# Kernel optimization log

Measured on AMD Instinct MI355X. Metric: run time of the kernel, lower is better.

## Reference

```python
import jax, jax.numpy as jnp
import numpy as np

NUM_NODES = 100
WINDOW = 128
GH = 256       # graph_hidden_channels
DH = 64        # discrepancy_hidden_channels
OUT = 128      # out_channels
B = 256        # graphs per batch
N = B * NUM_NODES
E = 409600


def _mconv(x, w, b):
    # x: [B, n, W], w: [n, 2, k], b: [n, 2]  (per-node Conv1d(1,2,k), 'same' padding)
    k = w.shape[-1]
    W = x.shape[-1]
    p = k // 2
    xp = jnp.pad(x, ((0, 0), (0, 0), (p, p)))
    win = jnp.stack([xp[..., j:j + W] for j in range(k)], axis=-1)  # [B,n,W,k]
    return jnp.einsum('bnwk,nck->bncw', win, w) + b[None, :, :, None]


def _gcn(x, edge_index, Wg, bg):
    # PyG GCNConv: add self-loops, symmetric normalization, then linear
    Nn = x.shape[0]
    xw = x @ Wg.T
    loops = jnp.arange(Nn, dtype=edge_index.dtype)
    src = jnp.concatenate([edge_index[0], loops])
    dst = jnp.concatenate([edge_index[1], loops])
    deg = jax.ops.segment_sum(jnp.ones(src.shape[0], dtype=xw.dtype), dst, num_segments=Nn)
    norm = jax.lax.rsqrt(jnp.maximum(deg, 1e-12))
    coef = norm[src] * norm[dst]
    agg = jax.ops.segment_sum(coef[:, None] * xw[src], dst, num_segments=Nn)
    return agg + bg


def setup_inputs() -> dict:
    key = jax.random.key(0)
    ks = jax.random.split(key, 20)
    f = 6 * WINDOW
    s = lambda d: 1.0 / np.sqrt(d)
    inp = {
        'x1': jax.random.normal(ks[0], (N, WINDOW), jnp.float32),
        'x2': jax.random.normal(ks[1], (N, WINDOW), jnp.float32),
        'edge_index1': jax.random.randint(ks[2], (2, E), 0, N, jnp.int32),
        'edge_index2': jax.random.randint(ks[3], (2, E), 0, N, jnp.int32),
        'w3': jax.random.normal(ks[4], (NUM_NODES, 2, 3), jnp.float32) * s(3),
        'b3': jax.random.normal(ks[5], (NUM_NODES, 2), jnp.float32) * s(3),
        'w5': jax.random.normal(ks[6], (NUM_NODES, 2, 5), jnp.float32) * s(5),
        'b5': jax.random.normal(ks[7], (NUM_NODES, 2), jnp.float32) * s(5),
        'w7': jax.random.normal(ks[8], (NUM_NODES, 2, 7), jnp.float32) * s(7),
        'b7': jax.random.normal(ks[9], (NUM_NODES, 2), jnp.float32) * s(7),
        'Wff': jax.random.normal(ks[10], (NUM_NODES, GH, f), jnp.float32) * s(f),
        'bff': jax.random.normal(ks[11], (NUM_NODES, GH), jnp.float32) * s(f),
        'Wg': jax.random.normal(ks[12], (GH, GH), jnp.float32) * s(GH),
        'bg': jax.random.normal(ks[13], (GH,), jnp.float32) * s(GH),
        'Wd': jax.random.normal(ks[14], (NUM_NODES, DH, 2 * GH), jnp.float32) * s(2 * GH),
        'bd': jax.random.normal(ks[15], (NUM_NODES, DH), jnp.float32) * s(2 * GH),
        'Wfc': jax.random.normal(ks[16], (OUT, NUM_NODES * DH), jnp.float32) * s(NUM_NODES * DH),
        'bfc': jax.random.normal(ks[17], (OUT,), jnp.float32) * s(NUM_NODES * DH),
    }
    return inp


def reference(x1, x2, edge_index1, edge_index2, w3, b3, w5, b5, w7, b7,
              Wff, bff, Wg, bg, Wd, bd, Wfc, bfc):
    n = w3.shape[0]
    Nn, W = x1.shape
    Bg = Nn // n

    def branch(x):
        xg = x.reshape(Bg, n, W)
        # multiscale CNN: concat conv3/conv5/conv7 along channel -> [B,n,6,W]
        c = jnp.concatenate([_mconv(xg, w3, b3), _mconv(xg, w5, b5), _mconv(xg, w7, b7)], axis=2)
        c = jax.nn.relu(c.reshape(Bg, n, 6 * W))            # channel-major flatten (matches view(-1))
        h = jax.nn.relu(jnp.einsum('bnf,nhf->bnh', c, Wff) + bff)
        return h.reshape(Nn, -1)

    h1 = jax.nn.relu(_gcn(branch(x1), edge_index1, Wg, bg))
    h2 = jax.nn.relu(_gcn(branch(x2), edge_index2, Wg, bg))
    H = h1.shape[-1]
    cat = jnp.concatenate([h1.reshape(Bg, n, H), h2.reshape(Bg, n, H)], axis=-1)  # [B,n,2H]
    d = jnp.einsum('bnf,ndf->bnd', cat, Wd) + bd            # per-node discrepancy FC
    du = jax.nn.relu(d.reshape(Bg, -1))                     # node-major -> [B, n*DH]
    return du @ Wfc.T + bfc
```

## Files before the change

kernel.cpp:

```cpp
#include <hip/hip_runtime.h>

#define DI __device__ __forceinline__

typedef __bf16 bf16_t;
typedef bf16_t bf16x8 __attribute__((ext_vector_type(8)));
typedef float f32x4 __attribute__((ext_vector_type(4)));
typedef ushort ushort8v __attribute__((ext_vector_type(8)));

static constexpr int NNODE = 100, WIN = 128, GH = 256, DH = 64, OUTC = 128, NB = 256;
static constexpr int NTOT = NB * NNODE;
static constexpr int NE = 409600;
static constexpr int FFK = 6 * WIN;
static constexpr size_t CB = (size_t)NNODE * NB * FFK;
static constexpr size_t HB = (size_t)NTOT * GH;
static constexpr int CVT_BLKS = 23264;

DI ushort f2bf(float f) {
  union { float f; unsigned u; } v; v.f = f;
  unsigned r = v.u + 0x7fffu + ((v.u >> 16) & 1u);
  return (ushort)(r >> 16);
}
DI float bf2f(ushort s) {
  union { unsigned u; float f; } v; v.u = ((unsigned)s) << 16; return v.f;
}

DI void gload16(const void* g, void* l) {
  __builtin_amdgcn_global_load_lds((const __attribute__((address_space(1))) void*)g,
                                   (__attribute__((address_space(3))) void*)l, 16, 0, 0);
}


DI void cvt_body(int bx, const float* s0, const float* s1, const float* s2, const float* s3,
                 ushort* d0, ushort* d1, ushort* d2, ushort* d3) {
  int j = bx * 256 + threadIdx.x;
  const float* s; ushort* d;
  if (j < 19660800 / 4) { s = s0; d = d0; }
  else if ((j -= 19660800 / 4) < 3276800 / 4) { s = s1; d = d1; }
  else if ((j -= 3276800 / 4) < 819200 / 4) { s = s2; d = d2; }
  else { j -= 819200 / 4; s = s3; d = d3; }
  float4 v = reinterpret_cast<const float4*>(s)[j];
  ushort4 o;
  o.x = f2bf(v.x); o.y = f2bf(v.y); o.z = f2bf(v.z); o.w = f2bf(v.w);
  reinterpret_cast<ushort4*>(d)[j] = o;
}

DI void hist_body(int bx, const int* d1, const int* d2, int* deg, int* rank) {
  int i = bx * 256 + threadIdx.x;
  if (i < NE) rank[i] = atomicAdd(&deg[d1[i]], 1);
  else if (i < 2 * NE) rank[i] = atomicAdd(&deg[NTOT + d2[i - NE]], 1);
}

DI void fill_body(int bx, const int* e1, const int* e2, const int* offs,
                  const int* rank, int* csr) {
  int i = bx * 256 + threadIdx.x;
  if (i < NE) {
    int d = e1[NE + i];
    csr[offs[d] + rank[i]] = e1[i];
  } else if (i < 2 * NE) {
    int ii = i - NE;
    int d = e2[NE + ii];
    csr[NE + offs[NTOT + 1 + d] + rank[i]] = e2[ii];
  }
}

DI void scan_body(int set, const int* deg_, int* offs_, float* norm_) {
  const int* deg = deg_ + set * NTOT;
  int* offs = offs_ + set * (NTOT + 1);
  float* norm = norm_ + set * NTOT;
  __shared__ int part[256];
  int t = threadIdx.x;
  int base = t * 100;
  int s = 0;
  for (int j = 0; j < 100; ++j) s += deg[base + j];
  part[t] = s;
  __syncthreads();
  for (int d = 1; d < 256; d <<= 1) {
    int vv = (t >= d) ? part[t - d] : 0;
    __syncthreads();
    part[t] += vv;
    __syncthreads();
  }
  int run = (t > 0) ? part[t - 1] : 0;
  for (int j = 0; j < 100; ++j) {
    int dv = deg[base + j];
    offs[base + j] = run;
    norm[base + j] = rsqrtf((float)(dv + 1));
    run += dv;
  }
  if (t == 255) offs[NTOT] = part[255];
}

DI void conv_body(int bx, const float* x1, const float* x2,
                  const float* w3, const float* b3, const float* w5, const float* b5,
                  const float* w7, const float* b7, ushort* c) {
  const int t = threadIdx.x;
  const int rowi = t >> 4;
  const int idx = t & 15;
  int r = bx * 16 + rowi;
  int br = r >= NTOT;
  int rr = r - br * NTOT;
  const float* x = br ? x2 : x1;
  int b = rr / 100, node = rr - b * 100;

  __shared__ float xs[16][136];
  const int w0 = idx * 8;
  float4 v0 = *reinterpret_cast<const float4*>(x + (size_t)rr * WIN + w0);
  float4 v1 = *reinterpret_cast<const float4*>(x + (size_t)rr * WIN + w0 + 4);
  *reinterpret_cast<float4*>(&xs[rowi][4 + w0]) = v0;
  *reinterpret_cast<float4*>(&xs[rowi][4 + w0 + 4]) = v1;
  if (idx == 0) { xs[rowi][0] = 0.f; xs[rowi][1] = 0.f; xs[rowi][2] = 0.f; xs[rowi][3] = 0.f; }
  if (idx == 15) { xs[rowi][132] = 0.f; xs[rowi][133] = 0.f; xs[rowi][134] = 0.f; xs[rowi][135] = 0.f; }
  __syncthreads();

  float xv[14];
#pragma unroll
  for (int j = 0; j < 14; ++j) xv[j] = xs[rowi][1 + w0 + j];

  const float* W3 = w3 + node * 6;  const float* B3 = b3 + node * 2;
  const float* W5 = w5 + node * 10; const float* B5 = b5 + node * 2;
  const float* W7 = w7 + node * 14; const float* B7 = b7 + node * 2;
  ushort* out = c + (size_t)br * CB + (size_t)(node * NB + b) * FFK + w0;

#pragma unroll
  for (int ch = 0; ch < 2; ++ch) {
    float k3[3], k5[5], k7[7];
#pragma unroll
    for (int j = 0; j < 3; ++j) k3[j] = W3[ch * 3 + j];
#pragma unroll
    for (int j = 0; j < 5; ++j) k5[j] = W5[ch * 5 + j];
#pragma unroll
    for (int j = 0; j < 7; ++j) k7[j] = W7[ch * 7 + j];
    float bb3 = B3[ch], bb5 = B5[ch], bb7 = B7[ch];
    ushort8v o3, o5, o7;
#pragma unroll
    for (int p = 0; p < 8; ++p) {
      float a3 = bb3, a5 = bb5, a7 = bb7;
#pragma unroll
      for (int j = 0; j < 3; ++j) a3 += k3[j] * xv[p + 2 + j];
#pragma unroll
      for (int j = 0; j < 5; ++j) a5 += k5[j] * xv[p + 1 + j];
#pragma unroll
      for (int j = 0; j < 7; ++j) a7 += k7[j] * xv[p + j];
      o3[p] = f2bf(fmaxf(a3, 0.f));
      o5[p] = f2bf(fmaxf(a5, 0.f));
      o7[p] = f2bf(fmaxf(a7, 0.f));
    }
    *reinterpret_cast<ushort8v*>(out + (0 + ch) * WIN) = o3;
    *reinterpret_cast<ushort8v*>(out + (2 + ch) * WIN) = o5;
    *reinterpret_cast<ushort8v*>(out + (4 + ch) * WIN) = o7;
  }
}

template <int MODE>
DI void gemm_body(int bx, int by, const ushort* __restrict__ A, const ushort* __restrict__ A2,
                  const ushort* __restrict__ Bm, ushort* __restrict__ obf,
                  float* __restrict__ of, const float* __restrict__ bias) {
  constexpr int BN = (MODE == 2) ? 64 : 128;
  constexpr int KT = (MODE == 0) ? 12 : (MODE == 1) ? 4 : (MODE == 2) ? 8 : 4;
  constexpr int LDA = (MODE == 0) ? 768 : (MODE == 1) ? 256 : (MODE == 2) ? 256 : 6400;
  constexpr int LDB = (MODE == 0) ? 768 : (MODE == 1) ? 256 : (MODE == 2) ? 512 : 6400;
  constexpr int MF = (MODE == 2) ? 2 : 4;
  constexpr int NF = 4;

  __shared__ ushort As[128 * 64];
  __shared__ ushort Bs[BN * 64];

  const int tid = threadIdx.x, wv = tid >> 6, lane = tid & 63;
  const int j8 = (((lane & 7) ^ (lane >> 3)) - (lane & 7)) * 8;

  int mt = 0, nt = 0, node = 0, kbase = 0, br = 0;
  if constexpr (MODE == 0) {
    int h = bx;
    int s = (h & 7) * 100 + (h >> 3);
    nt = s & 1; int rest = s >> 1;
    mt = rest & 1; int yy = rest >> 1;
    br = yy >= 100; node = yy - br * 100;
  } else if constexpr (MODE == 1) {
    int h = bx;
    int s = (h & 7) * 100 + (h >> 3);
    nt = s & 1; int rest = s >> 1;
    br = rest >= 200; mt = rest - br * 200;
  } else if constexpr (MODE == 2) { mt = bx; node = by; }
  else { mt = bx; kbase = by * 256; }

  const ushort* Ab = nullptr; const ushort* Bb = nullptr;
  if constexpr (MODE == 0) { Ab = A + (size_t)br * CB + (size_t)node * (NB * FFK) + (size_t)mt * 128 * FFK;
                             Bb = Bm + (size_t)node * (GH * FFK) + (size_t)nt * 128 * FFK; }
  else if constexpr (MODE == 1) { Ab = A + (size_t)br * HB + (size_t)mt * 128 * GH;
                                  Bb = Bm + (size_t)nt * 128 * GH; }
  else if constexpr (MODE == 2) { Bb = Bm + (size_t)node * (DH * 512); }
  else { Ab = A + (size_t)mt * 128 * 6400 + kbase; Bb = Bm + kbase; }

  const int wr = (MODE == 2) ? wv : (wv >> 1);
  const int wc = (MODE == 2) ? 0 : (wv & 1);

  f32x4 acc[MF][NF] = {};

  for (int kt = 0; kt < KT; ++kt) {
    const int k0 = kt * 64;
    __syncthreads();
#pragma unroll
    for (int it = 0; it < 4; ++it) {
      int rb = it * 32 + wv * 8;
      int row = rb + (lane >> 3);
      const ushort* gp;
      if constexpr (MODE == 2) {
        int b_ = mt * 128 + row;
        const ushort* src = (k0 < 256) ? A : A2;
        gp = src + (size_t)(b_ * NNODE + node) * GH + (k0 & 255) + (lane & 7) * 8 + j8;
      } else {
        gp = Ab + (size_t)row * LDA + k0 + (lane & 7) * 8 + j8;
      }
      gload16(gp, &As[rb * 64]);
    }
#pragma unroll
    for (int it = 0; it < BN / 32; ++it) {
      int rb = it * 32 + wv * 8;
      int row = rb + (lane >> 3);
      gload16(Bb + (size_t)row * LDB + k0 + (lane & 7) * 8 + j8, &Bs[rb * 64]);
    }
    __syncthreads();
#pragma unroll
    for (int kk = 0; kk < 2; ++kk) {
      const int ch8 = ((kk * 4 + (lane >> 4)) ^ (lane & 7)) * 8;
      bf16x8 af[MF], bfr[NF];
#pragma unroll
      for (int m = 0; m < MF; ++m) {
        int rr = wr * (MF * 16) + m * 16 + (lane & 15);
        af[m] = *reinterpret_cast<const bf16x8*>(&As[rr * 64 + ch8]);
      }
#pragma unroll
      for (int n = 0; n < NF; ++n) {
        int rr = wc * 64 + n * 16 + (lane & 15);
        bfr[n] = *reinterpret_cast<const bf16x8*>(&Bs[rr * 64 + ch8]);
      }
#pragma unroll
      for (int m = 0; m < MF; ++m)
#pragma unroll
        for (int n = 0; n < NF; ++n)
          acc[m][n] = __builtin_amdgcn_mfma_f32_16x16x32_bf16(af[m], bfr[n], acc[m][n], 0, 0, 0);
    }
  }

  const int lrow = (lane >> 4) * 4, lcol = lane & 15;
#pragma unroll
  for (int m = 0; m < MF; ++m) {
#pragma unroll
    for (int n = 0; n < NF; ++n) {
      int cc = wc * 64 + n * 16 + lcol;
#pragma unroll
      for (int rg = 0; rg < 4; ++rg) {
        int rr = wr * (MF * 16) + m * 16 + lrow + rg;
        float val = acc[m][n][rg];
        if constexpr (MODE == 0) {
          int b_ = mt * 128 + rr;
          int col = nt * 128 + cc;
          val = fmaxf(val + bias[node * GH + col], 0.f);
          obf[(size_t)br * HB + (size_t)(b_ * NNODE + node) * GH + col] = f2bf(val);
        } else if constexpr (MODE == 1) {
          int R = mt * 128 + rr;
          int col = nt * 128 + cc;
          obf[(size_t)br * HB + (size_t)R * GH + col] = f2bf(val * bias[br * NTOT + R]);
        } else if constexpr (MODE == 2) {
          int b_ = mt * 128 + rr;
          val = fmaxf(val + bias[node * DH + cc], 0.f);
          obf[(size_t)b_ * (NNODE * DH) + node * DH + cc] = f2bf(val);
        } else {
          int R = mt * 128 + rr;
          if (by == 0) val += bias[cc];
          atomicAdd(&of[R * OUTC + cc], val);
        }
      }
    }
  }
}


__global__ __launch_bounds__(256) void fused1_k(
    const float* __restrict__ Wff, const float* __restrict__ Wd,
    const float* __restrict__ Wfc, const float* __restrict__ Wg,
    ushort* __restrict__ Wffb, ushort* __restrict__ Wdb,
    ushort* __restrict__ Wfcb, ushort* __restrict__ Wgb,
    const int* __restrict__ e1d, const int* __restrict__ e2d,
    int* __restrict__ deg, int* __restrict__ rank,
    const float* __restrict__ x1, const float* __restrict__ x2,
    const float* __restrict__ w3, const float* __restrict__ b3,
    const float* __restrict__ w5, const float* __restrict__ b5,
    const float* __restrict__ w7, const float* __restrict__ b7,
    ushort* __restrict__ c) {
  int bx = blockIdx.x;
  if (bx < 3200) hist_body(bx, e1d, e2d, deg, rank);
  else if (bx < 6400) conv_body(bx - 3200, x1, x2, w3, b3, w5, b5, w7, b7, c);
  else cvt_body(bx - 6400, Wff, Wd, Wfc, Wg, Wffb, Wdb, Wfcb, Wgb);
}

__global__ __launch_bounds__(256) void scan_k(const int* __restrict__ deg,
                                              int* __restrict__ offs, float* __restrict__ nrm) {
  scan_body(blockIdx.x, deg, offs, nrm);
}

__global__ __launch_bounds__(256) void fused3_k(
    const ushort* __restrict__ cbuf, const ushort* __restrict__ Wffb,
    ushort* __restrict__ h, const float* __restrict__ bff,
    const int* __restrict__ e1, const int* __restrict__ e2,
    const int* __restrict__ offs, const int* __restrict__ rank, int* __restrict__ csr) {
  if ((int)blockIdx.x < 800)
    gemm_body<0>(blockIdx.x, 0, cbuf, nullptr, Wffb, h, nullptr, bff);
  else
    fill_body(blockIdx.x - 800, e1, e2, offs, rank, csr);
}

template <int MODE>
__global__ __launch_bounds__(256) void gemm_k(const ushort* __restrict__ A, const ushort* __restrict__ A2,
                                              const ushort* __restrict__ Bm, ushort* __restrict__ obf,
                                              float* __restrict__ of, const float* __restrict__ bias) {
  gemm_body<MODE>(blockIdx.x, blockIdx.y, A, A2, Bm, obf, of, bias);
}

__global__ __launch_bounds__(256) void agg_k(const ushort* __restrict__ xw_, const int* __restrict__ offs_,
                                             const int* __restrict__ csr_, const float* __restrict__ norm_,
                                             const float* __restrict__ bg, ushort* __restrict__ hg_) {
  int idx = blockIdx.x * 4 + (threadIdx.x >> 6);
  int br = idx >= NTOT;
  int v = idx - br * NTOT;
  const ushort* xw = xw_ + (size_t)br * HB;
  const int* offs = offs_ + br * (NTOT + 1);
  const int* csr = csr_ + br * NE;
  const float* norm = norm_ + br * NTOT;
  ushort* hg = hg_ + (size_t)br * HB;

  int lane = threadIdx.x & 63;
  int half = lane >> 5;
  int colb = (lane & 31) * 8;
  const ushort* base = xw + colb;

  float a[8] = {0.f, 0.f, 0.f, 0.f, 0.f, 0.f, 0.f, 0.f};
  if (half == 0) {
    ushort8v q = *reinterpret_cast<const ushort8v*>(base + (size_t)v * GH);
#pragma unroll
    for (int i = 0; i < 8; ++i) a[i] += bf2f(q[i]);
  }
  int e0 = offs[v], e1 = offs[v + 1];
  int j = e0 + half;
  for (; j + 6 < e1; j += 8) {
    int s0 = csr[j], s1 = csr[j + 2], s2 = csr[j + 4], s3 = csr[j + 6];
    ushort8v q0 = *reinterpret_cast<const ushort8v*>(base + (size_t)s0 * GH);
    ushort8v q1 = *reinterpret_cast<const ushort8v*>(base + (size_t)s1 * GH);
    ushort8v q2 = *reinterpret_cast<const ushort8v*>(base + (size_t)s2 * GH);
    ushort8v q3 = *reinterpret_cast<const ushort8v*>(base + (size_t)s3 * GH);
#pragma unroll
    for (int i = 0; i < 8; ++i)
      a[i] += (bf2f(q0[i]) + bf2f(q1[i])) + (bf2f(q2[i]) + bf2f(q3[i]));
  }
  for (; j + 2 < e1; j += 4) {
    int s0 = csr[j], s1 = csr[j + 2];
    ushort8v q0 = *reinterpret_cast<const ushort8v*>(base + (size_t)s0 * GH);
    ushort8v q1 = *reinterpret_cast<const ushort8v*>(base + (size_t)s1 * GH);
#pragma unroll
    for (int i = 0; i < 8; ++i) a[i] += bf2f(q0[i]) + bf2f(q1[i]);
  }
  if (j < e1) {
    int s0 = csr[j];
    ushort8v q0 = *reinterpret_cast<const ushort8v*>(base + (size_t)s0 * GH);
#pragma unroll
    for (int i = 0; i < 8; ++i) a[i] += bf2f(q0[i]);
  }
#pragma unroll
  for (int i = 0; i < 8; ++i) a[i] += __shfl_xor(a[i], 32);

  if (half == 0) {
    float nv = norm[v];
    float4 bb0 = *reinterpret_cast<const float4*>(bg + colb);
    float4 bb1 = *reinterpret_cast<const float4*>(bg + colb + 4);
    ushort8v o;
    o[0] = f2bf(fmaxf(nv * a[0] + bb0.x, 0.f));
    o[1] = f2bf(fmaxf(nv * a[1] + bb0.y, 0.f));
    o[2] = f2bf(fmaxf(nv * a[2] + bb0.z, 0.f));
    o[3] = f2bf(fmaxf(nv * a[3] + bb0.w, 0.f));
    o[4] = f2bf(fmaxf(nv * a[4] + bb1.x, 0.f));
    o[5] = f2bf(fmaxf(nv * a[5] + bb1.y, 0.f));
    o[6] = f2bf(fmaxf(nv * a[6] + bb1.z, 0.f));
    o[7] = f2bf(fmaxf(nv * a[7] + bb1.w, 0.f));
    *reinterpret_cast<ushort8v*>(hg + (size_t)v * GH + colb) = o;
  }
}

extern "C" void kernel_launch(void* const* d_in, const int* in_sizes, int n_in,
                              void* d_out, int out_size, void* d_ws, size_t ws_size,
                              hipStream_t stream) {
  const float* x1 = (const float*)d_in[0];
  const float* x2 = (const float*)d_in[1];
  const int* e1 = (const int*)d_in[2];
  const int* e2 = (const int*)d_in[3];
  const float* w3 = (const float*)d_in[4];  const float* b3 = (const float*)d_in[5];
  const float* w5 = (const float*)d_in[6];  const float* b5 = (const float*)d_in[7];
  const float* w7 = (const float*)d_in[8];  const float* b7 = (const float*)d_in[9];
  const float* Wff = (const float*)d_in[10]; const float* bff = (const float*)d_in[11];
  const float* Wg = (const float*)d_in[12];  const float* bg = (const float*)d_in[13];
  const float* Wd = (const float*)d_in[14];  const float* bd = (const float*)d_in[15];
  const float* Wfc = (const float*)d_in[16]; const float* bfc = (const float*)d_in[17];
  float* out = (float*)d_out;

  char* ws = (char*)d_ws;
  size_t off = 0;
  auto alloc = [&](size_t bytes) -> char* {
    char* p = ws + off;
    off = (off + bytes + 255) & ~(size_t)255;
    return p;
  };
  ushort* Wffb = (ushort*)alloc(19660800ull * 2);
  ushort* Wdb  = (ushort*)alloc(3276800ull * 2);
  ushort* Wfcb = (ushort*)alloc(819200ull * 2);
  ushort* Wgb  = (ushort*)alloc(65536ull * 2);
  ushort* cbuf = (ushort*)alloc(2 * CB * 2);
  ushort* h    = (ushort*)alloc(2 * HB * 2);
  ushort* xw   = (ushort*)alloc(2 * HB * 2);
  int* deg   = (int*)alloc(2 * NTOT * 4);
  int* offs  = (int*)alloc(2 * (NTOT + 1) * 4);
  int* rank  = (int*)alloc(2 * NE * 4);
  int* csr   = (int*)alloc(2 * NE * 4);
  float* nrm = (float*)alloc(2 * NTOT * 4);
  ushort* du = cbuf;

  hipMemsetAsync(deg, 0, 2 * NTOT * 4, stream);
  hipMemsetAsync(out, 0, (size_t)out_size * 4, stream);

  fused1_k<<<6400 + CVT_BLKS, 256, 0, stream>>>(Wff, Wd, Wfc, Wg, Wffb, Wdb, Wfcb, Wgb,
                                                e1 + NE, e2 + NE, deg, rank,
                                                x1, x2, w3, b3, w5, b5, w7, b7, cbuf);
  scan_k<<<2, 256, 0, stream>>>(deg, offs, nrm);
  fused3_k<<<4000, 256, 0, stream>>>(cbuf, Wffb, h, bff, e1, e2, offs, rank, csr);

  gemm_k<1><<<800, 256, 0, stream>>>(h, nullptr, Wgb, xw, nullptr, nrm);
  agg_k<<<12800, 256, 0, stream>>>(xw, offs, csr, nrm, bg, h);

  gemm_k<2><<<dim3(2, 100), 256, 0, stream>>>(h, h + HB, Wdb, du, nullptr, bd);
  gemm_k<3><<<dim3(2, 25), 256, 0, stream>>>(du, nullptr, Wfcb, nullptr, out, bfc);
}
```

Baseline: 264.8 us.

## Replace global-atomic degree histogram with segmented LDS histogram and segment scan

Edge destinations are split into 64 segments per graph. Each segment is counted in shared memory with packed 16-bit counters, which gives a local rank per edge. A new segscan kernel prefix-sums the per-segment counts into per-segment bases and per-node degrees, and the CSR fill adds offset, segment base and local rank. The aim is to remove roughly 819k contended global atomics and the degree memset. In exchange it adds several MB of segcnt/segbase traffic, an extra launch, and a 51 KB static LDS allocation that applies to every block of fused1_k, including the conv and conversion blocks, which may reduce their occupancy.

```diff
diff --git a/kernel.cpp b/kernel.cpp
--- a/kernel.cpp
+++ b/kernel.cpp
@@ -14,6 +14,8 @@
 static constexpr size_t CB = (size_t)NNODE * NB * FFK;
 static constexpr size_t HB = (size_t)NTOT * GH;
 static constexpr int CVT_BLKS = 23264;
+static constexpr int NSEG = 64, SEGE = NE / NSEG;
+static constexpr int NPK = NTOT / 2;
 
 DI ushort f2bf(float f) {
   union { float f; unsigned u; } v; v.f = f;
@@ -44,23 +46,41 @@
   reinterpret_cast<ushort4*>(d)[j] = o;
 }
 
-DI void hist_body(int bx, const int* d1, const int* d2, int* deg, int* rank) {
+DI void histseg_body(int bx, const int* e1d, const int* e2d,
+                     ushort* rank_local, uint* segcnt, uint* cnt ) {
+  int set = bx & 1, seg = bx >> 1;
+  int tid = threadIdx.x;
+#pragma unroll
+  for (int k = 0; k < NPK / 256; ++k) cnt[tid + k * 256] = 0;
+  __syncthreads();
+  const int* dstp = (set ? e2d : e1d) + seg * SEGE;
+  ushort* rl = rank_local + set * NE + seg * SEGE;
+#pragma unroll
+  for (int k = 0; k < SEGE / 256; ++k) {
+    int i = k * 256 + tid;
+    int d = dstp[i];
+    uint sh = (d & 1) * 16;
+    uint old = atomicAdd(&cnt[d >> 1], 1u << sh);
+    rl[i] = (ushort)((old >> sh) & 0xffffu);
+  }
+  __syncthreads();
+  uint* sc = segcnt + (size_t)(set * NSEG + seg) * NPK;
+#pragma unroll
+  for (int k = 0; k < NPK / 256; ++k) sc[tid + k * 256] = cnt[tid + k * 256];
+}
+
+DI void fill_body(int bx, const int* e1, const int* e2, const int* offs,
+                  const ushort* rank_local, const uint* segbase, int* csr) {
   int i = bx * 256 + threadIdx.x;
-  if (i < NE) rank[i] = atomicAdd(&deg[d1[i]], 1);
-  else if (i < 2 * NE) rank[i] = atomicAdd(&deg[NTOT + d2[i - NE]], 1);
-}
-
-DI void fill_body(int bx, const int* e1, const int* e2, const int* offs,
-                  const int* rank, int* csr) {
-  int i = bx * 256 + threadIdx.x;
-  if (i < NE) {
-    int d = e1[NE + i];
-    csr[offs[d] + rank[i]] = e1[i];
-  } else if (i < 2 * NE) {
-    int ii = i - NE;
-    int d = e2[NE + ii];
-    csr[NE + offs[NTOT + 1 + d] + rank[i]] = e2[ii];
-  }
+  int set = i >= NE;
+  int ii = i - set * NE;
+  const int* e = set ? e2 : e1;
+  int d = e[NE + ii];
+  int seg = ii / SEGE;
+  uint b32 = segbase[(size_t)(set * NSEG + seg) * NPK + (d >> 1)];
+  int base = (b32 >> ((d & 1) * 16)) & 0xffff;
+  int pos = offs[set * (NTOT + 1) + d] + base + rank_local[i];
+  csr[set * NE + pos] = e[ii];
 }
 
 DI void scan_body(int set, const int* deg_, int* offs_, float* norm_) {
@@ -92,7 +112,7 @@
 
 DI void conv_body(int bx, const float* x1, const float* x2,
                   const float* w3, const float* b3, const float* w5, const float* b5,
-                  const float* w7, const float* b7, ushort* c) {
+                  const float* w7, const float* b7, ushort* c, float* xs ) {
   const int t = threadIdx.x;
   const int rowi = t >> 4;
   const int idx = t & 15;
@@ -102,19 +122,19 @@
   const float* x = br ? x2 : x1;
   int b = rr / 100, node = rr - b * 100;
 
-  __shared__ float xs[16][136];
+  float* row = xs + rowi * 136;
   const int w0 = idx * 8;
   float4 v0 = *reinterpret_cast<const float4*>(x + (size_t)rr * WIN + w0);
   float4 v1 = *reinterpret_cast<const float4*>(x + (size_t)rr * WIN + w0 + 4);
-  *reinterpret_cast<float4*>(&xs[rowi][4 + w0]) = v0;
-  *reinterpret_cast<float4*>(&xs[rowi][4 + w0 + 4]) = v1;
-  if (idx == 0) { xs[rowi][0] = 0.f; xs[rowi][1] = 0.f; xs[rowi][2] = 0.f; xs[rowi][3] = 0.f; }
-  if (idx == 15) { xs[rowi][132] = 0.f; xs[rowi][133] = 0.f; xs[rowi][134] = 0.f; xs[rowi][135] = 0.f; }
+  *reinterpret_cast<float4*>(&row[4 + w0]) = v0;
+  *reinterpret_cast<float4*>(&row[4 + w0 + 4]) = v1;
+  if (idx == 0) { row[0] = 0.f; row[1] = 0.f; row[2] = 0.f; row[3] = 0.f; }
+  if (idx == 15) { row[132] = 0.f; row[133] = 0.f; row[134] = 0.f; row[135] = 0.f; }
   __syncthreads();
 
   float xv[14];
 #pragma unroll
-  for (int j = 0; j < 14; ++j) xv[j] = xs[rowi][1 + w0 + j];
+  for (int j = 0; j < 14; ++j) xv[j] = row[1 + w0 + j];
 
   const float* W3 = w3 + node * 6;  const float* B3 = b3 + node * 2;
   const float* W5 = w5 + node * 10; const float* B5 = b5 + node * 2;
@@ -282,16 +302,32 @@
     ushort* __restrict__ Wffb, ushort* __restrict__ Wdb,
     ushort* __restrict__ Wfcb, ushort* __restrict__ Wgb,
     const int* __restrict__ e1d, const int* __restrict__ e2d,
-    int* __restrict__ deg, int* __restrict__ rank,
+    ushort* __restrict__ rank_local, uint* __restrict__ segcnt,
     const float* __restrict__ x1, const float* __restrict__ x2,
     const float* __restrict__ w3, const float* __restrict__ b3,
     const float* __restrict__ w5, const float* __restrict__ b5,
     const float* __restrict__ w7, const float* __restrict__ b7,
     ushort* __restrict__ c) {
+  __shared__ uint smem[NPK];
   int bx = blockIdx.x;
-  if (bx < 3200) hist_body(bx, e1d, e2d, deg, rank);
-  else if (bx < 6400) conv_body(bx - 3200, x1, x2, w3, b3, w5, b5, w7, b7, c);
-  else cvt_body(bx - 6400, Wff, Wd, Wfc, Wg, Wffb, Wdb, Wfcb, Wgb);
+  if (bx < 128) histseg_body(bx, e1d, e2d, rank_local, segcnt, smem);
+  else if (bx < 3328) conv_body(bx - 128, x1, x2, w3, b3, w5, b5, w7, b7, c, (float*)smem);
+  else cvt_body(bx - 3328, Wff, Wd, Wfc, Wg, Wffb, Wdb, Wfcb, Wgb);
+}
+
+__global__ __launch_bounds__(256) void segscan_k(const uint* __restrict__ segcnt,
+                                                 uint* __restrict__ segbase, int* __restrict__ deg) {
+  int set = blockIdx.y;
+  int p = blockIdx.x * 256 + threadIdx.x;
+  uint lo = 0, hi = 0;
+  const uint* sc = segcnt + (size_t)set * NSEG * NPK + p;
+  uint* sb = segbase + (size_t)set * NSEG * NPK + p;
+  for (int s = 0; s < NSEG; ++s) {
+    uint v = sc[(size_t)s * NPK];
+    sb[(size_t)s * NPK] = lo | (hi << 16);
+    lo += v & 0xffffu; hi += v >> 16;
+  }
+  reinterpret_cast<int2*>(deg)[set * NPK + p] = make_int2((int)lo, (int)hi);
 }
 
 __global__ __launch_bounds__(256) void scan_k(const int* __restrict__ deg,
@@ -303,11 +339,12 @@
     const ushort* __restrict__ cbuf, const ushort* __restrict__ Wffb,
     ushort* __restrict__ h, const float* __restrict__ bff,
     const int* __restrict__ e1, const int* __restrict__ e2,
-    const int* __restrict__ offs, const int* __restrict__ rank, int* __restrict__ csr) {
+    const int* __restrict__ offs, const ushort* __restrict__ rank_local,
+    const uint* __restrict__ segbase, int* __restrict__ csr) {
   if ((int)blockIdx.x < 800)
     gemm_body<0>(blockIdx.x, 0, cbuf, nullptr, Wffb, h, nullptr, bff);
   else
-    fill_body(blockIdx.x - 800, e1, e2, offs, rank, csr);
+    fill_body(blockIdx.x - 800, e1, e2, offs, rank_local, segbase, csr);
 }
 
 template <int MODE>
@@ -415,21 +452,24 @@
   ushort* cbuf = (ushort*)alloc(2 * CB * 2);
   ushort* h    = (ushort*)alloc(2 * HB * 2);
   ushort* xw   = (ushort*)alloc(2 * HB * 2);
-  int* deg   = (int*)alloc(2 * NTOT * 4);
-  int* offs  = (int*)alloc(2 * (NTOT + 1) * 4);
-  int* rank  = (int*)alloc(2 * NE * 4);
-  int* csr   = (int*)alloc(2 * NE * 4);
-  float* nrm = (float*)alloc(2 * NTOT * 4);
+  int* deg     = (int*)alloc(2 * NTOT * 4);
+  int* offs    = (int*)alloc(2 * (NTOT + 1) * 4);
+  ushort* rankl = (ushort*)alloc(2 * NE * 2);
+  uint* segcnt  = (uint*)alloc((size_t)2 * NSEG * NPK * 4);
+  uint* segbase = (uint*)alloc((size_t)2 * NSEG * NPK * 4);
+  int* csr     = (int*)alloc(2 * NE * 4);
+  float* nrm   = (float*)alloc(2 * NTOT * 4);
   ushort* du = cbuf;
 
-  hipMemsetAsync(deg, 0, 2 * NTOT * 4, stream);
   hipMemsetAsync(out, 0, (size_t)out_size * 4, stream);
 
-  fused1_k<<<6400 + CVT_BLKS, 256, 0, stream>>>(Wff, Wd, Wfc, Wg, Wffb, Wdb, Wfcb, Wgb,
-                                                e1 + NE, e2 + NE, deg, rank,
-                                                x1, x2, w3, b3, w5, b5, w7, b7, cbuf);
+  fused1_k<<<128 + 3200 + CVT_BLKS, 256, 0, stream>>>(
+      Wff, Wd, Wfc, Wg, Wffb, Wdb, Wfcb, Wgb,
+      e1 + NE, e2 + NE, rankl, segcnt,
+      x1, x2, w3, b3, w5, b5, w7, b7, cbuf);
+  segscan_k<<<dim3(NPK / 256, 2), 256, 0, stream>>>(segcnt, segbase, deg);
   scan_k<<<2, 256, 0, stream>>>(deg, offs, nrm);
-  fused3_k<<<4000, 256, 0, stream>>>(cbuf, Wffb, h, bff, e1, e2, offs, rank, csr);
+  fused3_k<<<4000, 256, 0, stream>>>(cbuf, Wffb, h, bff, e1, e2, offs, rankl, segbase, csr);
 
   gemm_k<1><<<800, 256, 0, stream>>>(h, nullptr, Wgb, xw, nullptr, nrm);
   agg_k<<<12800, 256, 0, stream>>>(xw, offs, csr, nrm, bg, h);
```

Result: faster. 252.1 us (-4.8%).
